# Performance work log

Measured on AMD Instinct MI355X. Metric: run time of the kernel, lower is better.

Reference implementation:

```python
import jax, jax.numpy as jnp
import numpy as np

# Model hyperparameters (upscaled from the repo's shakespear config)
L, E, H, T, B, V = 6, 1024, 16, 1024, 4, 32000
HD = E // H          # head_size = 64
EPS = 1e-5


def layernorm(x, g, b):
    m = x.mean(-1, keepdims=True)
    v = ((x - m) ** 2).mean(-1, keepdims=True)
    return (x - m) / jnp.sqrt(v + EPS) * g + b


def setup_inputs() -> dict:
    key = jax.random.key(0)
    ks = jax.random.split(key, 24)
    s = 0.02
    n = lambda k, shp: (jax.random.normal(k, shp) * s).astype(jnp.float32)
    return {
        "idx": jax.random.randint(ks[0], (B, T), 0, V),
        "tok_emb": n(ks[1], (V, E)),
        "pos_emb": n(ks[2], (T, E)),
        # per-head q/k/v weights stacked: [L, E, H, HD]
        "Wq": n(ks[3], (L, E, H, HD)),
        "Wk": n(ks[4], (L, E, H, HD)),
        "Wv": n(ks[5], (L, E, H, HD)),
        "Wo": n(ks[6], (L, E, E)),
        "bo": jnp.zeros((L, E), jnp.float32),
        "W1": n(ks[7], (L, E, 4 * E)),
        "b1": jnp.zeros((L, 4 * E), jnp.float32),
        "W2": n(ks[8], (L, 4 * E, E)),
        "b2": jnp.zeros((L, E), jnp.float32),
        "ln1_g": jnp.ones((L, E), jnp.float32),
        "ln1_b": jnp.zeros((L, E), jnp.float32),
        "ln2_g": jnp.ones((L, E), jnp.float32),
        "ln2_b": jnp.zeros((L, E), jnp.float32),
        "lnf_g": jnp.ones((E,), jnp.float32),
        "lnf_b": jnp.zeros((E,), jnp.float32),
        "Wlm": n(ks[9], (E, V)),
        "blm": jnp.zeros((V,), jnp.float32),
    }


def reference(idx, tok_emb, pos_emb, Wq, Wk, Wv, Wo, bo, W1, b1, W2, b2,
              ln1_g, ln1_b, ln2_g, ln2_b, lnf_g, lnf_b, Wlm, blm):
    x = tok_emb[idx] + pos_emb[None, :T]            # [B,T,E]
    mask = jnp.tril(jnp.ones((T, T), bool))
    scale = HD ** -0.5
    for l in range(L):
        h = layernorm(x, ln1_g[l], ln1_b[l])
        q = jnp.einsum('bte,ehd->bhtd', h, Wq[l])
        k = jnp.einsum('bte,ehd->bhtd', h, Wk[l])
        v = jnp.einsum('bte,ehd->bhtd', h, Wv[l])
        # NOTE: source computes K @ Q^T (reversed from standard attention)
        wei = jnp.einsum('bhtd,bhsd->bhts', k, q) * scale
        wei = jnp.where(mask, wei, -jnp.inf)
        wei = jax.nn.softmax(wei, axis=-1)
        att = jnp.einsum('bhts,bhsd->bhtd', wei, v)  # [B,H,T,HD]
        att = att.transpose(0, 2, 1, 3).reshape(B, T, E)
        x = x + att @ Wo[l] + bo[l]
        h2 = layernorm(x, ln2_g[l], ln2_b[l])
        x = x + jax.nn.relu(h2 @ W1[l] + b1[l]) @ W2[l] + b2[l]
    x = layernorm(x, lnf_g, lnf_b)
    logits = x @ Wlm + blm                           # [B,T,V]
    return logits
```

## Files before the change

kernel.cpp:

```cpp
#include <hip/hip_runtime.h>


typedef __bf16 bf16;
typedef __attribute__((ext_vector_type(8))) __bf16 bf16x8;
typedef __attribute__((ext_vector_type(4))) __bf16 bf16x4;
typedef __attribute__((ext_vector_type(4))) float  f32x4;

#define LAYERS 6
#define EMB    1024
#define HEADS  16
#define HDIM   64
#define SEQ    1024
#define BATCH  4
#define VOCAB  32000
#define ROWS   (BATCH * SEQ)

#define AS1(p) ((__attribute__((address_space(1))) void*)(p))
#define AS3(p) ((__attribute__((address_space(3))) void*)(p))

__global__ void transpose_cvt(const float* __restrict__ in, bf16* __restrict__ out,
                              int K, int N)
{
    __shared__ float tile[32][33];
    int n0 = blockIdx.x * 32, k0 = blockIdx.y * 32;
    int tx = threadIdx.x, ty = threadIdx.y;
#pragma unroll
    for (int r = 0; r < 4; ++r)
        tile[ty + 8 * r][tx] = in[(size_t)(k0 + ty + 8 * r) * N + n0 + tx];
    __syncthreads();
#pragma unroll
    for (int r = 0; r < 4; ++r)
        out[(size_t)(n0 + ty + 8 * r) * K + k0 + tx] = (bf16)tile[tx][ty + 8 * r];
}

__global__ void transpose4_cvt(const float* __restrict__ s0, const float* __restrict__ s1,
                               const float* __restrict__ s2, const float* __restrict__ s3,
                               bf16* __restrict__ d0, bf16* __restrict__ d1,
                               bf16* __restrict__ d2, bf16* __restrict__ d3)
{
    const float* in; bf16* out;
    switch (blockIdx.z) {
        case 0: in = s0; out = d0; break;
        case 1: in = s1; out = d1; break;
        case 2: in = s2; out = d2; break;
        default: in = s3; out = d3; break;
    }
    __shared__ float tile[32][33];
    int n0 = blockIdx.x * 32, k0 = blockIdx.y * 32;
    int tx = threadIdx.x, ty = threadIdx.y;
#pragma unroll
    for (int r = 0; r < 4; ++r)
        tile[ty + 8 * r][tx] = in[(size_t)(k0 + ty + 8 * r) * 1024 + n0 + tx];
    __syncthreads();
#pragma unroll
    for (int r = 0; r < 4; ++r)
        out[(size_t)(n0 + ty + 8 * r) * 1024 + k0 + tx] = (bf16)tile[tx][ty + 8 * r];
}

__global__ void transpose_w12(const float* __restrict__ W1, const float* __restrict__ W2,
                              bf16* __restrict__ T1, bf16* __restrict__ T2)
{
    __shared__ float tile[32][33];
    int tx = threadIdx.x, ty = threadIdx.y;
    const float* in; bf16* out; int K, N, n0, k0;
    if (blockIdx.z == 0) { in = W1; out = T1; K = 1024; N = 4096;
                           n0 = blockIdx.x * 32; k0 = blockIdx.y * 32; }
    else                 { in = W2; out = T2; K = 4096; N = 1024;
                           n0 = blockIdx.y * 32; k0 = blockIdx.x * 32; }
#pragma unroll
    for (int r = 0; r < 4; ++r)
        tile[ty + 8 * r][tx] = in[(size_t)(k0 + ty + 8 * r) * N + n0 + tx];
    __syncthreads();
#pragma unroll
    for (int r = 0; r < 4; ++r)
        out[(size_t)(n0 + ty + 8 * r) * K + k0 + tx] = (bf16)tile[tx][ty + 8 * r];
}

__global__ void embed_kernel(const int* __restrict__ idx, const float* __restrict__ tok,
                             const float* __restrict__ pos, bf16* __restrict__ x)
{
    int row = blockIdx.x;
    int t   = row & (SEQ - 1);
    int id  = idx[row];
    int e   = threadIdx.x;
    float4 a = ((const float4*)(tok + (size_t)id * EMB))[e];
    float4 p = ((const float4*)(pos + (size_t)t  * EMB))[e];
    bf16x4 o;
    o.x = (bf16)(a.x + p.x); o.y = (bf16)(a.y + p.y);
    o.z = (bf16)(a.z + p.z); o.w = (bf16)(a.w + p.w);
    *(bf16x4*)(x + (size_t)row * EMB + e * 4) = o;
}

__global__ __launch_bounds__(256)
void ln_kernel(const bf16* __restrict__ x, const float* __restrict__ g,
               const float* __restrict__ b, bf16* __restrict__ out)
{
    int row = blockIdx.x;
    int t = threadIdx.x;
    bf16x4 xv = *(const bf16x4*)(x + (size_t)row * EMB + t * 4);
    float4 v; v.x = (float)xv.x; v.y = (float)xv.y; v.z = (float)xv.z; v.w = (float)xv.w;
    float s1 = v.x + v.y + v.z + v.w;
    float s2 = v.x * v.x + v.y * v.y + v.z * v.z + v.w * v.w;
#pragma unroll
    for (int off = 32; off > 0; off >>= 1) {
        s1 += __shfl_down(s1, off);
        s2 += __shfl_down(s2, off);
    }
    __shared__ float l1[4], l2[4];
    int wave = t >> 6;
    if ((t & 63) == 0) { l1[wave] = s1; l2[wave] = s2; }
    __syncthreads();
    float tot1 = l1[0] + l1[1] + l1[2] + l1[3];
    float tot2 = l2[0] + l2[1] + l2[2] + l2[3];
    float mean = tot1 * (1.f / EMB);
    float var  = tot2 * (1.f / EMB) - mean * mean;
    float rstd = rsqrtf(var + 1e-5f);
    float4 gg = ((const float4*)g)[t];
    float4 bb = ((const float4*)b)[t];
    bf16x4 o;
    o.x = (bf16)((v.x - mean) * rstd * gg.x + bb.x);
    o.y = (bf16)((v.y - mean) * rstd * gg.y + bb.y);
    o.z = (bf16)((v.z - mean) * rstd * gg.z + bb.z);
    o.w = (bf16)((v.w - mean) * rstd * gg.w + bb.w);
    *(bf16x4*)(out + (size_t)row * EMB + t * 4) = o;
}

template <int MODE>
__global__ __launch_bounds__(512, 1)
void gemm256_kernel(const bf16* __restrict__ A, const bf16* __restrict__ BT,
                    void* Cv, const float* __restrict__ bias,
                    int N, int K, int nbm, int nbn)
{
    __shared__ __align__(16) bf16 lds[2][2][256 * 64];
    const int tid  = threadIdx.x;
    const int wave = tid >> 6, lane = tid & 63;
    const int lo = lane & 15, hi = lane >> 4;
    const int wm = wave >> 2, wn = wave & 3;

    const int nwg = nbm * nbn;
    const int q = nwg >> 3, rem = nwg & 7;
    const int xcd = blockIdx.x & 7, boff = blockIdx.x >> 3;
    const int swz = (xcd < rem ? xcd * (q + 1) : rem * (q + 1) + (xcd - rem) * q) + boff;
    const int m0 = (swz % nbm) * 256;
    const int n0 = (swz / nbm) * 256;

    f32x4 acc[8][4];
#pragma unroll
    for (int m = 0; m < 8; ++m)
#pragma unroll
        for (int n = 0; n < 4; ++n)
            acc[m][n] = (f32x4){0.f, 0.f, 0.f, 0.f};

    const int NT = K >> 6;

    auto stage_ht = [&](int t, int ht) {
        const int slot = t & 1;
        const int k0 = t << 6;
        const int ab = ht >> 1;
        const int rbase = (ht & 1) << 7;
        const bf16* src = ab ? BT : A;
        const int base0 = ab ? n0 : m0;
#pragma unroll
        for (int j = 0; j < 2; ++j) {
            int g  = j * 512 + tid;
            int r  = g >> 3;
            int cc = (g & 7) ^ (r & 7);
            __builtin_amdgcn_global_load_lds(
                AS1(src + (size_t)(base0 + rbase + r) * K + k0 + cc * 8),
                AS3((char*)&lds[slot][ab][rbase * 64] + (size_t)g * 16), 16, 0, 0);
        }
    };

    bf16x8 bcur[4][2], bnxt[4][2], ae[2][2], ao[2][2];

    auto lda = [&](int t, int mp, bf16x8 (&out)[2][2]) {
        const int slot = t & 1;
#pragma unroll
        for (int mi = 0; mi < 2; ++mi)
#pragma unroll
            for (int ks = 0; ks < 2; ++ks) {
                int r = wm * 128 + (mp * 2 + mi) * 16 + lo;
                int pos = (ks * 4 + hi) ^ (r & 7);
                out[mi][ks] = *(const bf16x8*)(&lds[slot][0][r * 64 + pos * 8]);
            }
    };
    auto ldb = [&](int t, bf16x8 (&out)[4][2]) {
        const int slot = t & 1;
#pragma unroll
        for (int n = 0; n < 4; ++n)
#pragma unroll
            for (int ks = 0; ks < 2; ++ks) {
                int r = wn * 64 + n * 16 + lo;
                int pos = (ks * 4 + hi) ^ (r & 7);
                out[n][ks] = *(const bf16x8*)(&lds[slot][1][r * 64 + pos * 8]);
            }
    };
    auto mfma16 = [&](int mp, bf16x8 (&a)[2][2]) {
        __builtin_amdgcn_s_setprio(1);
#pragma unroll
        for (int mi = 0; mi < 2; ++mi)
#pragma unroll
            for (int n = 0; n < 4; ++n)
#pragma unroll
                for (int ks = 0; ks < 2; ++ks)
                    acc[mp * 2 + mi][n] =
                        __builtin_amdgcn_mfma_f32_16x16x32_bf16(a[mi][ks], bcur[n][ks],
                                                                acc[mp * 2 + mi][n], 0, 0, 0);
        __builtin_amdgcn_s_setprio(0);
    };

    stage_ht(0, 0); stage_ht(0, 1); stage_ht(0, 2); stage_ht(0, 3);
    asm volatile("s_waitcnt vmcnt(0)\n\ts_barrier" ::: "memory");
    ldb(0, bcur);
    lda(0, 0, ae);

    for (int t = 0; t < NT; ++t) {
        const bool more = (t + 1 < NT);
        if (more) { stage_ht(t + 1, 0); stage_ht(t + 1, 1); }
        lda(t, 1, ao);
        mfma16(0, ae);
        if (more) { stage_ht(t + 1, 2); stage_ht(t + 1, 3); }
        lda(t, 2, ae);
        mfma16(1, ao);
        lda(t, 3, ao);
        mfma16(2, ae);
        if (more) {
            asm volatile("s_waitcnt vmcnt(0) lgkmcnt(0)\n\ts_barrier" ::: "memory");
            ldb(t + 1, bnxt);
            lda(t + 1, 0, ae);
        }
        mfma16(3, ao);
        if (more) {
#pragma unroll
            for (int n = 0; n < 4; ++n)
#pragma unroll
                for (int ks = 0; ks < 2; ++ks)
                    bcur[n][ks] = bnxt[n][ks];
        }
    }

#pragma unroll
    for (int m = 0; m < 8; ++m) {
        int row = m0 + wm * 128 + m * 16 + hi * 4;
#pragma unroll
        for (int n = 0; n < 4; ++n) {
            int col = n0 + wn * 64 + n * 16 + lo;
            float bv = (MODE != 0) ? bias[col] : 0.f;
#pragma unroll
            for (int j = 0; j < 4; ++j) {
                size_t o = (size_t)(row + j) * N + col;
                float v = acc[m][n][j] + bv;
                if (MODE == 2)      ((bf16*)Cv)[o]  = (bf16)fmaxf(v, 0.f);
                else if (MODE == 3) ((float*)Cv)[o] = v;
                else                ((bf16*)Cv)[o]  = (bf16)v;
            }
        }
    }
}

template <int MODE>
__global__ __launch_bounds__(256)
void gemm_kernel(const bf16* __restrict__ A, const bf16* __restrict__ BT,
                 void* Cv, const float* __restrict__ bias,
                 const bf16* __restrict__ resid, int N, int K)
{
    __shared__ __align__(16) bf16 As[128 * 64];
    __shared__ __align__(16) bf16 Bs[128 * 64];
    const int tid = threadIdx.x;
    const int wave = tid >> 6, lane = tid & 63;
    const int lo = lane & 15, hi = lane >> 4;
    const int wm = wave >> 1, wn = wave & 1;
    const int m0 = blockIdx.y * 128, n0 = blockIdx.x * 128;

    f32x4 acc[4][4];
#pragma unroll
    for (int m = 0; m < 4; ++m)
#pragma unroll
        for (int n = 0; n < 4; ++n)
            acc[m][n] = (f32x4){0.f, 0.f, 0.f, 0.f};

    const int sb = wave * 4;
    for (int k0 = 0; k0 < K; k0 += 64) {
#pragma unroll
        for (int i = 0; i < 4; ++i) {
            int g   = (sb + i) * 64 + lane;
            int row = g >> 3;
            int lc  = (g & 7) ^ (row & 7);
            const bf16* ga = A  + (size_t)(m0 + row) * K + k0 + lc * 8;
            const bf16* gb = BT + (size_t)(n0 + row) * K + k0 + lc * 8;
            __builtin_amdgcn_global_load_lds(AS1(ga), AS3(As + (sb + i) * 512), 16, 0, 0);
            __builtin_amdgcn_global_load_lds(AS1(gb), AS3(Bs + (sb + i) * 512), 16, 0, 0);
        }
        asm volatile("s_waitcnt vmcnt(0)" ::: "memory");
        __syncthreads();
#pragma unroll
        for (int ks = 0; ks < 2; ++ks) {
            bf16x8 af[4], bfr[4];
#pragma unroll
            for (int m = 0; m < 4; ++m) {
                int r  = wm * 64 + m * 16 + lo;
                int pc = (ks * 4 + hi) ^ (r & 7);
                af[m] = *(const bf16x8*)(As + r * 64 + pc * 8);
            }
#pragma unroll
            for (int n = 0; n < 4; ++n) {
                int r  = wn * 64 + n * 16 + lo;
                int pc = (ks * 4 + hi) ^ (r & 7);
                bfr[n] = *(const bf16x8*)(Bs + r * 64 + pc * 8);
            }
#pragma unroll
            for (int m = 0; m < 4; ++m)
#pragma unroll
                for (int n = 0; n < 4; ++n)
                    acc[m][n] = __builtin_amdgcn_mfma_f32_16x16x32_bf16(af[m], bfr[n], acc[m][n], 0, 0, 0);
        }
        __syncthreads();
    }

#pragma unroll
    for (int m = 0; m < 4; ++m) {
        int rbase = m0 + wm * 64 + m * 16 + hi * 4;
#pragma unroll
        for (int n = 0; n < 4; ++n) {
            int col = n0 + wn * 64 + n * 16 + lo;
            float bv = (MODE != 0) ? bias[col] : 0.f;
#pragma unroll
            for (int j = 0; j < 4; ++j) {
                size_t off = (size_t)(rbase + j) * N + col;
                float v = acc[m][n][j] + bv;
                if (MODE == 1)      ((bf16*)Cv)[off] = (bf16)(v + (float)resid[off]);
                else if (MODE == 2) ((bf16*)Cv)[off] = (bf16)fmaxf(v, 0.f);
                else if (MODE == 3) ((float*)Cv)[off] = v;
                else                ((bf16*)Cv)[off]  = (bf16)v;
            }
        }
    }
}

__global__ void vtrans_kernel(const bf16* __restrict__ qkv, bf16* __restrict__ vt)
{
    int bh = blockIdx.x; int b = bh >> 4, h = bh & 15;
    int t0 = blockIdx.y * 64;
    __shared__ bf16 tile[64][68];
    int tx = threadIdx.x, ty = threadIdx.y;
#pragma unroll
    for (int r = 0; r < 16; ++r) {
        int t = r * 4 + ty;
        tile[t][tx] = qkv[(size_t)(b * SEQ + t0 + t) * 3072 + 2048 + h * 64 + tx];
    }
    __syncthreads();
#pragma unroll
    for (int r = 0; r < 16; ++r) {
        int d = r * 4 + ty;
        vt[((size_t)bh * 64 + d) * SEQ + t0 + tx] = tile[tx][d];
    }
}

__global__ __launch_bounds__(64)
void attn_kernel(const bf16* __restrict__ qkv, const bf16* __restrict__ vt,
                 bf16* __restrict__ att)
{
    int bh = blockIdx.x; int b = bh >> 4, h = bh & 15;
    int t0 = blockIdx.y * 16;
    int lane = threadIdx.x;
    int lo = lane & 15, hi = lane >> 4;
    const bf16* kb = qkv + (size_t)(b * SEQ) * 3072 + EMB + h * 64;
    const bf16* qb = qkv + (size_t)(b * SEQ) * 3072 + h * 64;
    const bf16* vb = vt + (size_t)bh * 64 * SEQ;

    bf16x8 bK0 = *(const bf16x8*)(kb + (size_t)(t0 + lo) * 3072 + hi * 8);
    bf16x8 bK1 = *(const bf16x8*)(kb + (size_t)(t0 + lo) * 3072 + 32 + hi * 8);

    f32x4 o[4];
#pragma unroll
    for (int n = 0; n < 4; ++n) o[n] = (f32x4){0.f, 0.f, 0.f, 0.f};
    float mrun = -1e30f, lrun = 0.f;

    __shared__ __align__(16) bf16 plds[16][72];

    const int nt = (t0 + 16 + 63) >> 6;
    const int nfull = (t0 >= 64) ? (((t0 - 63) >> 6) + 1) : 0;

    auto tile_body = [&](int s0, bool masked) {
        f32x4 sc[4];
#pragma unroll
        for (int sh = 0; sh < 4; ++sh) sc[sh] = (f32x4){0.f, 0.f, 0.f, 0.f};
#pragma unroll
        for (int sh = 0; sh < 4; ++sh) {
            const bf16* qr = qb + (size_t)(s0 + sh * 16 + lo) * 3072;
            bf16x8 aQ0 = *(const bf16x8*)(qr + hi * 8);
            bf16x8 aQ1 = *(const bf16x8*)(qr + 32 + hi * 8);
            sc[sh] = __builtin_amdgcn_mfma_f32_16x16x32_bf16(aQ0, bK0, sc[sh], 0, 0, 0);
            sc[sh] = __builtin_amdgcn_mfma_f32_16x16x32_bf16(aQ1, bK1, sc[sh], 0, 0, 0);
        }
        const int tt = t0 + lo;
        float p[16];
        float mx = -1e30f;
#pragma unroll
        for (int sh = 0; sh < 4; ++sh)
#pragma unroll
            for (int j = 0; j < 4; ++j) {
                float val = sc[sh][j] * 0.125f;
                if (masked) {
                    int s = s0 + sh * 16 + hi * 4 + j;
                    if (s > tt) val = -1e30f;
                }
                p[sh * 4 + j] = val;
                mx = fmaxf(mx, val);
            }
        mx = fmaxf(mx, __shfl_xor(mx, 16));
        mx = fmaxf(mx, __shfl_xor(mx, 32));
        float mnew = fmaxf(mrun, mx);
        float scl = __expf(mrun - mnew);
        mrun = mnew;
        float rs = 0.f;
#pragma unroll
        for (int i = 0; i < 16; ++i) { p[i] = __expf(p[i] - mnew); rs += p[i]; }
        rs += __shfl_xor(rs, 16);
        rs += __shfl_xor(rs, 32);
        lrun = lrun * scl + rs;
        float sclj[4];
#pragma unroll
        for (int j = 0; j < 4; ++j) sclj[j] = __shfl(scl, hi * 4 + j);
#pragma unroll
        for (int n = 0; n < 4; ++n)
#pragma unroll
            for (int j = 0; j < 4; ++j)
                o[n][j] *= sclj[j];
        __syncthreads();
#pragma unroll
        for (int sh = 0; sh < 4; ++sh) {
            bf16x4 w;
            w.x = (bf16)p[sh * 4 + 0]; w.y = (bf16)p[sh * 4 + 1];
            w.z = (bf16)p[sh * 4 + 2]; w.w = (bf16)p[sh * 4 + 3];
            *(bf16x4*)(&plds[lo][sh * 16 + hi * 4]) = w;
        }
        __syncthreads();
        bf16x8 aP0 = *(const bf16x8*)(&plds[lo][hi * 8]);
        bf16x8 aP1 = *(const bf16x8*)(&plds[lo][32 + hi * 8]);
#pragma unroll
        for (int n = 0; n < 4; ++n) {
            bf16x8 bV0 = *(const bf16x8*)(vb + (size_t)(n * 16 + lo) * SEQ + s0 + hi * 8);
            bf16x8 bV1 = *(const bf16x8*)(vb + (size_t)(n * 16 + lo) * SEQ + s0 + 32 + hi * 8);
            o[n] = __builtin_amdgcn_mfma_f32_16x16x32_bf16(aP0, bV0, o[n], 0, 0, 0);
            o[n] = __builtin_amdgcn_mfma_f32_16x16x32_bf16(aP1, bV1, o[n], 0, 0, 0);
        }
    };

    for (int it = 0; it < nfull; ++it) tile_body(it * 64, false);
    for (int it = nfull; it < nt; ++it) tile_body(it * 64, true);

    float lj[4];
#pragma unroll
    for (int j = 0; j < 4; ++j) lj[j] = __shfl(lrun, hi * 4 + j);
#pragma unroll
    for (int j = 0; j < 4; ++j) {
        float inv = 1.f / lj[j];
        size_t rowoff = (size_t)(b * SEQ + t0 + hi * 4 + j) * EMB + h * 64;
#pragma unroll
        for (int n = 0; n < 4; ++n)
            att[rowoff + n * 16 + lo] = (bf16)(o[n][j] * inv);
    }
}

extern "C" void kernel_launch(void* const* d_in, const int* in_sizes, int n_in,
                              void* d_out, int out_size, void* d_ws, size_t ws_size,
                              hipStream_t stream)
{
    const int*   idx  = (const int*)d_in[0];
    const float* tok  = (const float*)d_in[1];
    const float* pos  = (const float*)d_in[2];
    const float* Wq   = (const float*)d_in[3];
    const float* Wk   = (const float*)d_in[4];
    const float* Wv   = (const float*)d_in[5];
    const float* Wo   = (const float*)d_in[6];
    const float* bo   = (const float*)d_in[7];
    const float* W1   = (const float*)d_in[8];
    const float* b1   = (const float*)d_in[9];
    const float* W2   = (const float*)d_in[10];
    const float* b2   = (const float*)d_in[11];
    const float* ln1g = (const float*)d_in[12];
    const float* ln1b = (const float*)d_in[13];
    const float* ln2g = (const float*)d_in[14];
    const float* ln2b = (const float*)d_in[15];
    const float* lnfg = (const float*)d_in[16];
    const float* lnfb = (const float*)d_in[17];
    const float* Wlm  = (const float*)d_in[18];
    const float* blm  = (const float*)d_in[19];
    float* out = (float*)d_out;

    char* ws = (char*)d_ws;
    size_t off = 0;
    auto alloc = [&](size_t bytes) { void* p = ws + off; off += (bytes + 255) & ~(size_t)255; return p; };
    bf16* x     = (bf16*)alloc((size_t)ROWS * EMB * 2);
    bf16* h     = (bf16*)alloc((size_t)ROWS * EMB * 2);
    bf16* qkv   = (bf16*)alloc((size_t)ROWS * 3072 * 2);
    bf16* vt    = (bf16*)alloc((size_t)ROWS * EMB * 2);
    bf16* attb  = (bf16*)alloc((size_t)ROWS * EMB * 2);
    bf16* mlp   = (bf16*)alloc((size_t)ROWS * 4096 * 2);
    bf16* WTqkv = (bf16*)alloc((size_t)3072 * 1024 * 2);
    bf16* WTo   = (bf16*)alloc((size_t)1024 * 1024 * 2);
    bf16* WT1   = (bf16*)alloc((size_t)4096 * 1024 * 2);
    bf16* WT2   = (bf16*)alloc((size_t)1024 * 4096 * 2);
    bf16* WTlm  = (bf16*)alloc((size_t)VOCAB * 1024 * 2);

    dim3 tb(32, 8);

    transpose_cvt<<<dim3(VOCAB / 32, 32), tb, 0, stream>>>(Wlm, WTlm, 1024, VOCAB);

    embed_kernel<<<ROWS, 256, 0, stream>>>(idx, tok, pos, x);

    for (int l = 0; l < LAYERS; ++l) {
        const size_t wqs = (size_t)l * 1024 * 1024;
        const size_t w14 = (size_t)l * 4096 * 1024;
        transpose4_cvt<<<dim3(32, 32, 4), tb, 0, stream>>>(
            Wq + wqs, Wk + wqs, Wv + wqs, Wo + wqs,
            WTqkv, WTqkv + (size_t)1024 * 1024, WTqkv + (size_t)2048 * 1024, WTo);
        transpose_w12<<<dim3(128, 32, 2), tb, 0, stream>>>(W1 + w14, W2 + w14, WT1, WT2);

        ln_kernel<<<ROWS, 256, 0, stream>>>(x, ln1g + l * EMB, ln1b + l * EMB, h);
        gemm256_kernel<0><<<16 * 12, 512, 0, stream>>>(h, WTqkv, qkv, nullptr, 3072, 1024, 16, 12);
        vtrans_kernel<<<dim3(64, 16), dim3(64, 4), 0, stream>>>(qkv, vt);
        attn_kernel<<<dim3(64, 64), 64, 0, stream>>>(qkv, vt, attb);
        gemm_kernel<1><<<dim3(8, 32), 256, 0, stream>>>(attb, WTo, x, bo + l * EMB, x, 1024, 1024);
        ln_kernel<<<ROWS, 256, 0, stream>>>(x, ln2g + l * EMB, ln2b + l * EMB, h);
        gemm256_kernel<2><<<16 * 16, 512, 0, stream>>>(h, WT1, mlp, b1 + l * 4096, 4096, 1024, 16, 16);
        gemm_kernel<1><<<dim3(8, 32), 256, 0, stream>>>(mlp, WT2, x, b2 + l * EMB, x, 1024, 4096);
    }
    ln_kernel<<<ROWS, 256, 0, stream>>>(x, lnfg, lnfb, h);
    gemm256_kernel<3><<<16 * 125, 512, 0, stream>>>(h, WTlm, out, blm, 32000, 1024, 16, 125);
}
```

Before: 2.094 ms.

## Fuse V transpose into QKV GEMM epilogue and drop vtrans kernel

The QKV projection moves from the 256-tile GEMM to the 128-tile gemm_kernel with a new MODE 4. Blocks covering the V columns write their output transposed straight into the vt buffer, so the separate vtrans_kernel launch and its extra read and write of V are gone. The cost is switching QKV to the smaller-tile GEMM, which may have lower throughput. The transposed stores are also 4-element strided writes along the sequence dimension, which coalesce worse.

New measurement: 2.095 ms. About the same (+0.0%).

```diff
diff --git a/kernel.cpp b/kernel.cpp
--- a/kernel.cpp
+++ b/kernel.cpp
@@ -262,7 +262,8 @@
 __global__ __launch_bounds__(256)
 void gemm_kernel(const bf16* __restrict__ A, const bf16* __restrict__ BT,
                  void* Cv, const float* __restrict__ bias,
-                 const bf16* __restrict__ resid, int N, int K)
+                 const bf16* __restrict__ resid, bf16* __restrict__ vt,
+                 int N, int K)
 {
     __shared__ __align__(16) bf16 As[128 * 64];
     __shared__ __align__(16) bf16 Bs[128 * 64];
@@ -317,42 +318,38 @@
         __syncthreads();
     }
 
+    if (MODE == 4 && n0 >= 2048) {
+#pragma unroll
+        for (int m = 0; m < 4; ++m) {
+            int rowb = m0 + wm * 64 + m * 16 + hi * 4;
+            int bb = rowb >> 10, t = rowb & 1023;
+#pragma unroll
+            for (int n = 0; n < 4; ++n) {
+                int hd = n0 - 2048 + wn * 64 + n * 16 + lo;
+                bf16x4 w;
+                w.x = (bf16)acc[m][n][0]; w.y = (bf16)acc[m][n][1];
+                w.z = (bf16)acc[m][n][2]; w.w = (bf16)acc[m][n][3];
+                *(bf16x4*)(vt + ((size_t)(bb * 1024 + hd)) * SEQ + t) = w;
+            }
+        }
+        return;
+    }
+
 #pragma unroll
     for (int m = 0; m < 4; ++m) {
         int rbase = m0 + wm * 64 + m * 16 + hi * 4;
 #pragma unroll
         for (int n = 0; n < 4; ++n) {
             int col = n0 + wn * 64 + n * 16 + lo;
-            float bv = (MODE != 0) ? bias[col] : 0.f;
+            float bv = (MODE == 1) ? bias[col] : 0.f;
 #pragma unroll
             for (int j = 0; j < 4; ++j) {
                 size_t off = (size_t)(rbase + j) * N + col;
                 float v = acc[m][n][j] + bv;
                 if (MODE == 1)      ((bf16*)Cv)[off] = (bf16)(v + (float)resid[off]);
-                else if (MODE == 2) ((bf16*)Cv)[off] = (bf16)fmaxf(v, 0.f);
-                else if (MODE == 3) ((float*)Cv)[off] = v;
-                else                ((bf16*)Cv)[off]  = (bf16)v;
-            }
-        }
-    }
-}
-
-__global__ void vtrans_kernel(const bf16* __restrict__ qkv, bf16* __restrict__ vt)
-{
-    int bh = blockIdx.x; int b = bh >> 4, h = bh & 15;
-    int t0 = blockIdx.y * 64;
-    __shared__ bf16 tile[64][68];
-    int tx = threadIdx.x, ty = threadIdx.y;
-#pragma unroll
-    for (int r = 0; r < 16; ++r) {
-        int t = r * 4 + ty;
-        tile[t][tx] = qkv[(size_t)(b * SEQ + t0 + t) * 3072 + 2048 + h * 64 + tx];
-    }
-    __syncthreads();
-#pragma unroll
-    for (int r = 0; r < 16; ++r) {
-        int d = r * 4 + ty;
-        vt[((size_t)bh * 64 + d) * SEQ + t0 + tx] = tile[tx][d];
+                else                ((bf16*)Cv)[off] = (bf16)v;
+            }
+        }
     }
 }
 
@@ -519,13 +516,12 @@
         transpose_w12<<<dim3(128, 32, 2), tb, 0, stream>>>(W1 + w14, W2 + w14, WT1, WT2);
 
         ln_kernel<<<ROWS, 256, 0, stream>>>(x, ln1g + l * EMB, ln1b + l * EMB, h);
-        gemm256_kernel<0><<<16 * 12, 512, 0, stream>>>(h, WTqkv, qkv, nullptr, 3072, 1024, 16, 12);
-        vtrans_kernel<<<dim3(64, 16), dim3(64, 4), 0, stream>>>(qkv, vt);
+        gemm_kernel<4><<<dim3(24, 32), 256, 0, stream>>>(h, WTqkv, qkv, nullptr, nullptr, vt, 3072, 1024);
         attn_kernel<<<dim3(64, 64), 64, 0, stream>>>(qkv, vt, attb);
-        gemm_kernel<1><<<dim3(8, 32), 256, 0, stream>>>(attb, WTo, x, bo + l * EMB, x, 1024, 1024);
+        gemm_kernel<1><<<dim3(8, 32), 256, 0, stream>>>(attb, WTo, x, bo + l * EMB, x, nullptr, 1024, 1024);
         ln_kernel<<<ROWS, 256, 0, stream>>>(x, ln2g + l * EMB, ln2b + l * EMB, h);
         gemm256_kernel<2><<<16 * 16, 512, 0, stream>>>(h, WT1, mlp, b1 + l * 4096, 4096, 1024, 16, 16);
-        gemm_kernel<1><<<dim3(8, 32), 256, 0, stream>>>(mlp, WT2, x, b2 + l * EMB, x, 1024, 4096);
+        gemm_kernel<1><<<dim3(8, 32), 256, 0, stream>>>(mlp, WT2, x, b2 + l * EMB, x, nullptr, 1024, 4096);
     }
     ln_kernel<<<ROWS, 256, 0, stream>>>(x, lnfg, lnfb, h);
     gemm256_kernel<3><<<16 * 125, 512, 0, stream>>>(h, WTlm, out, blm, 32000, 1024, 16, 125);
```
